# Kernel optimization log

Hardware: AMD Instinct MI355X
Metric: run time of the kernel (lower is better)

Reference implementation:

```python
import jax, jax.numpy as jnp
import numpy as np

NTYPES = 2
MAXNEI = 128      # maxNeighborNum
M2 = 16
NPER = 256        # atoms per type
B = 4
EMB = [25, 50, 100]
FIT_IN = M2 * EMB[-1]  # 1600
FH = 240


def setup_inputs() -> dict:
    key = jax.random.key(0)
    ks = jax.random.split(key, 16)
    s = 0.1
    inp = {
        "Ri": jax.random.normal(ks[0], (B, NTYPES * NPER, NTYPES * MAXNEI, 4), jnp.float32),
        "emb_W0": jax.random.normal(ks[1], (4, 1, EMB[0]), jnp.float32) * s,
        "emb_b0": jax.random.normal(ks[2], (4, EMB[0]), jnp.float32) * s,
        "emb_W1": jax.random.normal(ks[3], (4, EMB[0], EMB[1]), jnp.float32) * s,
        "emb_b1": jax.random.normal(ks[4], (4, EMB[1]), jnp.float32) * s,
        "emb_W2": jax.random.normal(ks[5], (4, EMB[1], EMB[2]), jnp.float32) * s,
        "emb_b2": jax.random.normal(ks[6], (4, EMB[2]), jnp.float32) * s,
        "fit_W0": jax.random.normal(ks[7], (2, FIT_IN, FH), jnp.float32) * 0.02,
        "fit_b0": jax.random.normal(ks[8], (2, FH), jnp.float32) * s,
        "fit_W1": jax.random.normal(ks[9], (2, FH, FH), jnp.float32) * 0.05,
        "fit_b1": jax.random.normal(ks[10], (2, FH), jnp.float32) * s,
        "fit_W2": jax.random.normal(ks[11], (2, FH, FH), jnp.float32) * 0.05,
        "fit_b2": jax.random.normal(ks[12], (2, FH), jnp.float32) * s,
        "fit_W3": jax.random.normal(ks[13], (2, FH, 1), jnp.float32) * 0.05,
        "fit_b3": jax.random.normal(ks[14], (2, 1), jnp.float32),
    }
    return inp


def _emb(s, W0, b0, W1, b1, W2, b2):
    # DeepMD-style embedding MLP with doubling resnet skips (1->25->50->100)
    h0 = jnp.tanh(s @ W0 + b0)
    h1 = jnp.tanh(h0 @ W1 + b1) + jnp.concatenate([h0, h0], axis=-1)
    h2 = jnp.tanh(h1 @ W2 + b2) + jnp.concatenate([h1, h1], axis=-1)
    return h2


def _fit(d, W0, b0, W1, b1, W2, b2, W3, b3):
    h = jnp.tanh(d @ W0 + b0)
    h = jnp.tanh(h @ W1 + b1) + h   # resnet skip (equal dims)
    h = jnp.tanh(h @ W2 + b2) + h
    return h @ W3 + b3              # [B, N, 1]


def reference(Ri, emb_W0, emb_b0, emb_W1, emb_b1, emb_W2, emb_b2,
              fit_W0, fit_b0, fit_W1, fit_b1, fit_W2, fit_b2, fit_W3, fit_b3):
    type_nums = NTYPES
    Ei_blocks = []
    for i in range(NTYPES):                      # center-atom type
        Ri_i = Ri[:, i * NPER:(i + 1) * NPER]    # [B, NPER, NTYPES*M, 4]
        xyz = None
        for j in range(NTYPES):                  # neighbor type
            blk = Ri_i[:, :, j * MAXNEI:(j + 1) * MAXNEI, :]  # [B,N,M,4]
            S = blk[..., 0:1]                                  # [B,N,M,1]
            e = i * NTYPES + j
            G = _emb(S, emb_W0[e], emb_b0[e], emb_W1[e], emb_b1[e],
                     emb_W2[e], emb_b2[e])                     # [B,N,M,100]
            tmp = jnp.einsum('bnmc,bnmg->bncg', blk, G)        # [B,N,4,100]
            xyz = tmp if xyz is None else xyz + tmp
        xyz = xyz / (MAXNEI * type_nums)
        xyz_b = xyz[..., :M2]                                  # [B,N,4,16]
        DR = jnp.einsum('bncg,bnch->bngh', xyz, xyz_b)         # [B,N,100,16]
        DR = DR.reshape(B, NPER, FIT_IN)
        Ei_i = _fit(DR, fit_W0[i], fit_b0[i], fit_W1[i], fit_b1[i],
                    fit_W2[i], fit_b2[i], fit_W3[i], fit_b3[i])  # [B,N,1]
        Ei_blocks.append(Ei_i)
    Ei = jnp.concatenate(Ei_blocks, axis=1)     # [B, natoms_sum, 1]
    return Ei[..., 0]                            # per-atom energies [B, natoms_sum]
```

## Files before the change

### kernel.cpp

```cpp
#include <hip/hip_runtime.h>
#include <hip/hip_bf16.h>

#define FH 240
#define FIT_IN 1600
#define NK 2048
#define TLO -16.0f
#define TINVH 64.0f
#define KSPLIT0 8
#define CHUNK0 200

typedef _Float16 h8 __attribute__((ext_vector_type(8)));
typedef float f4v __attribute__((ext_vector_type(4)));

__device__ __forceinline__ float fast_tanh(float x) {
    float e2 = __builtin_amdgcn_exp2f(x * 2.8853900817779268f);
    return 1.0f - 2.0f * __builtin_amdgcn_rcpf(e2 + 1.0f);
}

#define FMA_ROW(r, s) \
    acc[r][0] += (s) * b0.x; acc[r][1] += (s) * b0.y; \
    acc[r][2] += (s) * b0.z; acc[r][3] += (s) * b0.w; \
    acc[r][4] += (s) * b1.x; acc[r][5] += (s) * b1.y; \
    acc[r][6] += (s) * b1.z; acc[r][7] += (s) * b1.w;

#define TOFF_W0   0
#define TOFF_B0   28
#define TOFF_B1   56
#define TOFF_B2   108
#define TOFF_W1   208
#define TOFF_W2   1508
#define TOFF_H0T  6708
#define TOFF_H1T  10008
#define TSMEM     16608

__global__ __launch_bounds__(256) void k_prep(
    const float* __restrict__ eW0, const float* __restrict__ eB0,
    const float* __restrict__ eW1, const float* __restrict__ eB1,
    const float* __restrict__ eW2, const float* __restrict__ eB2,
    float* __restrict__ T,
    const float* __restrict__ fW0, const float* __restrict__ fW1,
    const float* __restrict__ fW2,
    _Float16* __restrict__ W0T, _Float16* __restrict__ W1T,
    _Float16* __restrict__ W2T)
{
    __shared__ float sm[TSMEM];
    const int t = threadIdx.x;

    if (blockIdx.x >= 64) {
        const int bid0 = blockIdx.x - 64;
        const int total = 768000 + 115200 + 115200;
        for (int idx = bid0 * 256 + t; idx < total; idx += 448 * 256) {
            if (idx < 768000) {
                const int tp = idx / 384000, r = idx - tp * 384000;
                const int n = r / 1600, k = r - n * 1600;
                W0T[idx] = (_Float16)fW0[tp * 384000 + k * 240 + n];
            } else if (idx < 883200) {
                const int j = idx - 768000;
                const int tp = j / 57600, r = j - tp * 57600;
                const int n = r / 240, k = r - n * 240;
                W1T[j] = (_Float16)fW1[tp * 57600 + k * 240 + n];
            } else {
                const int j = idx - 883200;
                const int tp = j / 57600, r = j - tp * 57600;
                const int n = r / 240, k = r - n * 240;
                W2T[j] = (_Float16)fW2[tp * 57600 + k * 240 + n];
            }
        }
        return;
    }

    const int w    = t >> 6;
    const int lane = t & 63;
    const int mi   = lane & 7;
    const int gi   = lane >> 3;
    const int mrow = w * 32 + mi * 4;

    const int e  = blockIdx.x >> 4;
    const int k0 = (blockIdx.x & 15) * 128;

    for (int idx = t; idx < 1250; idx += 256) {
        int k = idx / 50, g = idx - k * 50;
        sm[TOFF_W1 + k * 52 + g] = eW1[e * 1250 + idx];
    }
    for (int idx = t; idx < 5000; idx += 256) {
        int k = idx / 100, r = idx - k * 100;
        int half = r / 50, g = r - half * 50;
        sm[TOFF_W2 + k * 104 + half * 52 + g] = eW2[e * 5000 + idx];
    }
    if (t < 25)       { sm[TOFF_W0 + t] = eW0[e * 25 + t]; sm[TOFF_B0 + t] = eB0[e * 25 + t]; }
    else if (t < 75)  { sm[TOFF_B1 + (t - 25)] = eB1[e * 50 + (t - 25)]; }
    else if (t < 175) { sm[TOFF_B2 + (t - 75)] = eB2[e * 100 + (t - 75)]; }
    __syncthreads();

    if (t < 128) {
        const float S = TLO + (float)(k0 + t) * (1.0f / TINVH);
        #pragma unroll
        for (int k = 0; k < 25; ++k)
            sm[TOFF_H0T + k * 132 + t] = fast_tanh(S * sm[TOFF_W0 + k] + sm[TOFF_B0 + k]);
    }
    __syncthreads();

    {
        float acc[4][8];
        #pragma unroll
        for (int r = 0; r < 4; ++r)
            #pragma unroll
            for (int c = 0; c < 8; ++c) acc[r][c] = 0.f;

        #pragma unroll 5
        for (int k = 0; k < 25; ++k) {
            const float4 av = *(const float4*)&sm[TOFF_H0T + k * 132 + mrow];
            const float4 b0 = *(const float4*)&sm[TOFF_W1 + k * 52 + gi * 8];
            const float4 b1 = *(const float4*)&sm[TOFF_W1 + k * 52 + gi * 8 + 4];
            FMA_ROW(0, av.x) FMA_ROW(1, av.y) FMA_ROW(2, av.z) FMA_ROW(3, av.w)
        }
        #pragma unroll
        for (int c = 0; c < 8; ++c) {
            const int g = gi * 8 + c;
            if (g < 50) {
                const int gm = (g < 25) ? g : g - 25;
                const float4 h0r = *(const float4*)&sm[TOFF_H0T + gm * 132 + mrow];
                const float bias = sm[TOFF_B1 + g];
                float4 o;
                o.x = fast_tanh(acc[0][c] + bias) + h0r.x;
                o.y = fast_tanh(acc[1][c] + bias) + h0r.y;
                o.z = fast_tanh(acc[2][c] + bias) + h0r.z;
                o.w = fast_tanh(acc[3][c] + bias) + h0r.w;
                *(float4*)&sm[TOFF_H1T + g * 132 + mrow] = o;
            }
        }
    }
    __syncthreads();

    for (int half = 0; half < 2; ++half) {
        float acc[4][8];
        #pragma unroll
        for (int r = 0; r < 4; ++r)
            #pragma unroll
            for (int c = 0; c < 8; ++c) acc[r][c] = 0.f;

        #pragma unroll 5
        for (int k = 0; k < 50; ++k) {
            const float4 av = *(const float4*)&sm[TOFF_H1T + k * 132 + mrow];
            const float4 b0 = *(const float4*)&sm[TOFF_W2 + k * 104 + half * 52 + gi * 8];
            const float4 b1 = *(const float4*)&sm[TOFF_W2 + k * 104 + half * 52 + gi * 8 + 4];
            FMA_ROW(0, av.x) FMA_ROW(1, av.y) FMA_ROW(2, av.z) FMA_ROW(3, av.w)
        }
        #pragma unroll
        for (int c = 0; c < 8; ++c) {
            const int g = gi * 8 + c;
            if (g < 50) {
                const float4 h1r = *(const float4*)&sm[TOFF_H1T + g * 132 + mrow];
                const float bias = sm[TOFF_B2 + half * 50 + g];
                float* out = T + ((size_t)e * NK + k0 + mrow) * 100 + half * 50 + g;
                out[0]   = fast_tanh(acc[0][c] + bias) + h1r.x;
                out[100] = fast_tanh(acc[1][c] + bias) + h1r.y;
                out[200] = fast_tanh(acc[2][c] + bias) + h1r.z;
                out[300] = fast_tanh(acc[3][c] + bias) + h1r.w;
            }
        }
    }
}

__global__ __launch_bounds__(256) void k_xyz(
    const float* __restrict__ Ri, const float* __restrict__ T,
    _Float16* __restrict__ DRh)
{
    __shared__ float4 sR[256];
    __shared__ float  sF[256];
    __shared__ int    sI[256];
    __shared__ float  sXYZ[400];

    const int t   = threadIdx.x;
    const int blk = blockIdx.x;
    const int b   = blk >> 9;
    const int i   = (blk >> 8) & 1;
    const int n   = blk & 255;

    for (int idx = t; idx < 400; idx += 256) sXYZ[idx] = 0.f;

    {
        const int jj = t >> 7, m = t & 127;
        const size_t row = ((size_t)(b * 512 + i * 256 + n)) * 256 + jj * 128 + m;
        const float4 r = *(const float4*)(Ri + row * 4);
        sR[t] = r;
        float u = (r.x - TLO) * TINVH;
        int ii = (int)u;
        ii = (ii < 0) ? 0 : ((ii > NK - 2) ? NK - 2 : ii);
        sI[t] = ii;
        sF[t] = u - (float)ii;
    }
    __syncthreads();

    const int jj = t >> 7;
    const int g  = t & 127;
    if (g < 100) {
        const float* Te = T + ((size_t)(i * 2 + jj)) * NK * 100 + g;
        float a0 = 0.f, a1 = 0.f, a2 = 0.f, a3 = 0.f;
        #pragma unroll 4
        for (int m = 0; m < 128; ++m) {
            const int s = jj * 128 + m;
            const float4 R = sR[s];
            const float  f = sF[s];
            const float* p = Te + (size_t)sI[s] * 100;
            const float v0 = p[0], v1 = p[100];
            const float G = v0 + f * (v1 - v0);
            a0 += R.x * G; a1 += R.y * G; a2 += R.z * G; a3 += R.w * G;
        }
        atomicAdd(&sXYZ[g],       a0);
        atomicAdd(&sXYZ[100 + g], a1);
        atomicAdd(&sXYZ[200 + g], a2);
        atomicAdd(&sXYZ[300 + g], a3);
    }
    __syncthreads();

    const float inv = 1.0f / 65536.0f;
    _Float16* dr = DRh + (((size_t)i * 4 + b) * 256 + n) * FIT_IN;
    for (int q = t; q < 400; q += 256) {
        const int gg = q >> 2, h0 = (q & 3) * 4;
        ushort4 pk;
        _Float16* ph = (_Float16*)&pk;
        #pragma unroll
        for (int r = 0; r < 4; ++r) {
            const int h = h0 + r;
            const float v = (sXYZ[gg] * sXYZ[h] + sXYZ[100 + gg] * sXYZ[100 + h]
                           + sXYZ[200 + gg] * sXYZ[200 + h] + sXYZ[300 + gg] * sXYZ[300 + h]) * inv;
            ph[r] = (_Float16)v;
        }
        *(ushort4*)(dr + gg * 16 + h0) = pk;
    }
}

template<int K, int CHUNK>
__global__ __launch_bounds__(256) void k_fit_mfma(
    const _Float16* __restrict__ A, const _Float16* __restrict__ WT,
    float* __restrict__ P)
{
    __shared__ _Float16 sA[64 * 40];
    __shared__ _Float16 sBT[240 * 40];

    const int t    = threadIdx.x;
    const int w    = t >> 6;
    const int lane = t & 63;
    const int ln   = lane & 15;
    const int quad = lane >> 4;

    const int mtile = blockIdx.x;
    const int ks    = blockIdx.y;
    const int row0  = mtile * 64;
    const int tp    = mtile >> 4;
    const int kbeg  = ks * CHUNK;
    const int kend  = (kbeg + CHUNK < K) ? (kbeg + CHUNK) : K;
    const int nf0   = w * 4;
    const int nfrags = (w < 3) ? 4 : 3;

    f4v acc[4][4];
    #pragma unroll
    for (int mf = 0; mf < 4; ++mf)
        #pragma unroll
        for (int nf = 0; nf < 4; ++nf) acc[mf][nf] = (f4v)0.f;

    const _Float16* Ab = A + (size_t)row0 * K;
    const _Float16* Wb = WT + (size_t)tp * 240 * K;

    for (int k0 = kbeg; k0 < kend; k0 += 32) {
        #pragma unroll
        for (int q = t; q < 512; q += 256) {
            const int m = q >> 3, kq = (q & 7) * 4;
            const int k = k0 + kq;
            uint2 v = make_uint2(0u, 0u);
            if (k < kend) v = *(const uint2*)(Ab + (size_t)m * K + k);
            *(uint2*)&sA[m * 40 + kq] = v;
        }
        for (int q = t; q < 1920; q += 256) {
            const int n = q >> 3, kq = (q & 7) * 4;
            const int k = k0 + kq;
            uint2 v = make_uint2(0u, 0u);
            if (k < kend) v = *(const uint2*)(Wb + (size_t)n * K + k);
            *(uint2*)&sBT[n * 40 + kq] = v;
        }
        __syncthreads();

        h8 afr[4];
        #pragma unroll
        for (int mf = 0; mf < 4; ++mf)
            afr[mf] = *(const h8*)&sA[(mf * 16 + ln) * 40 + quad * 8];
        #pragma unroll
        for (int nf = 0; nf < 4; ++nf) {
            if (nf < nfrags) {
                const h8 bfr = *(const h8*)&sBT[((nf0 + nf) * 16 + ln) * 40 + quad * 8];
                #pragma unroll
                for (int mf = 0; mf < 4; ++mf)
                    acc[mf][nf] = __builtin_amdgcn_mfma_f32_16x16x32_f16(
                        afr[mf], bfr, acc[mf][nf], 0, 0, 0);
            }
        }
        __syncthreads();
    }

    float* Pb = P + ((size_t)ks * 2048 + row0) * FH;
    #pragma unroll
    for (int nf = 0; nf < 4; ++nf) {
        if (nf < nfrags) {
            const int col = (nf0 + nf) * 16 + ln;
            #pragma unroll
            for (int mf = 0; mf < 4; ++mf)
                #pragma unroll
                for (int r = 0; r < 4; ++r) {
                    const int row = mf * 16 + quad * 4 + r;
                    Pb[(size_t)row * FH + col] = acc[mf][nf][r];
                }
        }
    }
}

__global__ __launch_bounds__(256) void k_fit_tail(
    const float* __restrict__ P,
    const _Float16* __restrict__ W1T, const _Float16* __restrict__ W2T,
    const float* __restrict__ fb0, const float* __restrict__ fb1,
    const float* __restrict__ fb2, const float* __restrict__ fW3,
    const float* __restrict__ fb3, float* __restrict__ out)
{
    __shared__ float    hRes[2][16 * 240];
    __shared__ _Float16 sA[16 * 264];
    __shared__ _Float16 sB[240 * 40];

    const int t    = threadIdx.x;
    const int w    = t >> 6;
    const int lane = t & 63;
    const int ln   = lane & 15;
    const int quad = lane >> 4;
    const int r0   = blockIdx.x * 16;
    const int tp   = r0 >> 10;
    const int nf0  = w * 4;
    const int nfrags = (w < 3) ? 4 : 3;

    #pragma unroll
    for (int j = 0; j < 15; ++j) {
        const int e = t + j * 256;
        const int m = e / 240, col = e - m * 240;
        const size_t base = (size_t)(r0 + m) * FH + col;
        float s = 0.f;
        #pragma unroll
        for (int ks = 0; ks < KSPLIT0; ++ks)
            s += P[(size_t)ks * 2048 * FH + base];
        const float v = fast_tanh(s + fb0[tp * FH + col]);
        hRes[0][m * 240 + col] = v;
        sA[m * 264 + col] = (_Float16)v;
    }
    if (t < 256) {
        const int m = t >> 4, c = 240 + (t & 15);
        sA[m * 264 + c] = (_Float16)0.f;
    }

    #pragma unroll
    for (int layer = 0; layer < 2; ++layer) {
        const _Float16* Wt = (layer == 0 ? W1T : W2T) + (size_t)tp * FH * FH;
        const float* Bias  = (layer == 0 ? fb1 : fb2) + tp * FH;
        const float* res   = hRes[layer];
        float* outb        = hRes[layer ^ 1];

        f4v acc[4];
        #pragma unroll
        for (int nf = 0; nf < 4; ++nf) acc[nf] = (f4v)0.f;

        for (int k0 = 0; k0 < 256; k0 += 32) {
            __syncthreads();
            for (int q = t; q < 1920; q += 256) {
                const int n = q >> 3, kq = (q & 7) * 4;
                const int k = k0 + kq;
                uint2 v = make_uint2(0u, 0u);
                if (k < FH) v = *(const uint2*)(Wt + (size_t)n * FH + k);
                *(uint2*)&sB[n * 40 + kq] = v;
            }
            __syncthreads();
            const h8 afr = *(const h8*)&sA[ln * 264 + k0 + quad * 8];
            #pragma unroll
            for (int nf = 0; nf < 4; ++nf) {
                if (nf < nfrags) {
                    const h8 bfr = *(const h8*)&sB[((nf0 + nf) * 16 + ln) * 40 + quad * 8];
                    acc[nf] = __builtin_amdgcn_mfma_f32_16x16x32_f16(afr, bfr, acc[nf], 0, 0, 0);
                }
            }
        }
        __syncthreads();

        #pragma unroll
        for (int nf = 0; nf < 4; ++nf) {
            if (nf < nfrags) {
                const int col = (nf0 + nf) * 16 + ln;
                const float bias = Bias[col];
                #pragma unroll
                for (int r = 0; r < 4; ++r) {
                    const int m = quad * 4 + r;
                    const float v = fast_tanh(acc[nf][r] + bias) + res[m * 240 + col];
                    outb[m * 240 + col] = v;
                    if (layer == 0) sA[m * 264 + col] = (_Float16)v;
                }
            }
        }
        __syncthreads();
    }

    const float* h2 = hRes[0];
    const float* wv = fW3 + tp * FH;
    #pragma unroll
    for (int rr = 0; rr < 4; ++rr) {
        const int m = w * 4 + rr;
        float s = 0.f;
        for (int k = lane; k < FH; k += 64)
            s += h2[m * 240 + k] * wv[k];
        #pragma unroll
        for (int off = 32; off > 0; off >>= 1) s += __shfl_down(s, off);
        if (lane == 0) {
            const int gr = r0 + m;
            const int b = (gr >> 8) & 3, n = gr & 255;
            out[b * 512 + tp * 256 + n] = s + fb3[tp];
        }
    }
}

extern "C" void kernel_launch(void* const* d_in, const int* in_sizes, int n_in,
                              void* d_out, int out_size, void* d_ws, size_t ws_size,
                              hipStream_t stream)
{
    const float* Ri  = (const float*)d_in[0];
    const float* eW0 = (const float*)d_in[1];
    const float* eB0 = (const float*)d_in[2];
    const float* eW1 = (const float*)d_in[3];
    const float* eB1 = (const float*)d_in[4];
    const float* eW2 = (const float*)d_in[5];
    const float* eB2 = (const float*)d_in[6];
    const float* fW0 = (const float*)d_in[7];
    const float* fb0 = (const float*)d_in[8];
    const float* fW1 = (const float*)d_in[9];
    const float* fb1 = (const float*)d_in[10];
    const float* fW2 = (const float*)d_in[11];
    const float* fb2 = (const float*)d_in[12];
    const float* fW3 = (const float*)d_in[13];
    const float* fb3 = (const float*)d_in[14];

    char* p = (char*)d_ws;
    float* T   = (float*)p;                 p += (size_t)4 * NK * 100 * 4;
    float* P   = (float*)p;                 p += (size_t)KSPLIT0 * 2048 * FH * 4;
    _Float16* DRh = (_Float16*)p;           p += (size_t)2048 * FIT_IN * 2;
    _Float16* W0T = (_Float16*)p;           p += (size_t)768000 * 2;
    _Float16* W1T = (_Float16*)p;           p += (size_t)115200 * 2;
    _Float16* W2T = (_Float16*)p;           p += (size_t)115200 * 2;

    k_prep<<<dim3(512), dim3(256), 0, stream>>>(eW0, eB0, eW1, eB1, eW2, eB2, T,
                                                fW0, fW1, fW2, W0T, W1T, W2T);
    k_xyz<<<dim3(2048), dim3(256), 0, stream>>>(Ri, T, DRh);

    k_fit_mfma<FIT_IN, CHUNK0><<<dim3(32, KSPLIT0), dim3(256), 0, stream>>>(DRh, W0T, P);

    k_fit_tail<<<dim3(128), dim3(256), 0, stream>>>(P, W1T, W2T, fb0, fb1, fb2, fW3, fb3,
                                                    (float*)d_out);
}
```

Measured before the change: 190.6 us.

## Stage whole K-chunk in LDS for fit GEMM and restructure tail layers

The first fitting-layer GEMM now loads its entire K chunk (96 wide) of activations and weights into shared memory once and then runs all MFMAs with no per-step barriers, with the split-K factor raised to 17 to keep the grid wide. The tail kernel stages weight rows in 64-row panels covering the full K dimension, so each wave computes one 16-column fragment over all of K. It also double-buffers the fp16 activations and keeps a single in-place fp32 residual. This trades fewer barriers and load phases for more LDS use and more partial-sum buffers for the tail to reduce.

```diff
diff --git a/kernel.cpp b/kernel.cpp
--- a/kernel.cpp
+++ b/kernel.cpp
@@ -6,8 +6,8 @@
 #define NK 2048
 #define TLO -16.0f
 #define TINVH 64.0f
-#define KSPLIT0 8
-#define CHUNK0 200
+#define KSPLIT0 17
+#define CHUNK0 96
 
 typedef _Float16 h8 __attribute__((ext_vector_type(8)));
 typedef float f4v __attribute__((ext_vector_type(4)));
@@ -231,13 +231,12 @@
     }
 }
 
-template<int K, int CHUNK>
 __global__ __launch_bounds__(256) void k_fit_mfma(
     const _Float16* __restrict__ A, const _Float16* __restrict__ WT,
     float* __restrict__ P)
 {
-    __shared__ _Float16 sA[64 * 40];
-    __shared__ _Float16 sBT[240 * 40];
+    __shared__ _Float16 sW[240 * 104];
+    __shared__ _Float16 sA[64 * 104];
 
     const int t    = threadIdx.x;
     const int w    = t >> 6;
@@ -249,10 +248,26 @@
     const int ks    = blockIdx.y;
     const int row0  = mtile * 64;
     const int tp    = mtile >> 4;
-    const int kbeg  = ks * CHUNK;
-    const int kend  = (kbeg + CHUNK < K) ? (kbeg + CHUNK) : K;
+    const int kbeg  = ks * CHUNK0;
+    const int kend  = (kbeg + CHUNK0 < FIT_IN) ? (kbeg + CHUNK0) : FIT_IN;
+    const int klen  = kend - kbeg;
     const int nf0   = w * 4;
     const int nfrags = (w < 3) ? 4 : 3;
+
+    const _Float16* Ab = A + (size_t)row0 * FIT_IN + kbeg;
+    const _Float16* Wb = WT + (size_t)tp * 240 * FIT_IN + kbeg;
+
+    for (int q = t; q < 240 * 24; q += 256) {
+        const int n = q / 24, kq = (q - n * 24) * 4;
+        if (kq < klen)
+            *(uint2*)&sW[n * 104 + kq] = *(const uint2*)(Wb + (size_t)n * FIT_IN + kq);
+    }
+    for (int q = t; q < 64 * 24; q += 256) {
+        const int m = q / 24, kq = (q - m * 24) * 4;
+        if (kq < klen)
+            *(uint2*)&sA[m * 104 + kq] = *(const uint2*)(Ab + (size_t)m * FIT_IN + kq);
+    }
+    __syncthreads();
 
     f4v acc[4][4];
     #pragma unroll
@@ -260,42 +275,21 @@
         #pragma unroll
         for (int nf = 0; nf < 4; ++nf) acc[mf][nf] = (f4v)0.f;
 
-    const _Float16* Ab = A + (size_t)row0 * K;
-    const _Float16* Wb = WT + (size_t)tp * 240 * K;
-
-    for (int k0 = kbeg; k0 < kend; k0 += 32) {
-        #pragma unroll
-        for (int q = t; q < 512; q += 256) {
-            const int m = q >> 3, kq = (q & 7) * 4;
-            const int k = k0 + kq;
-            uint2 v = make_uint2(0u, 0u);
-            if (k < kend) v = *(const uint2*)(Ab + (size_t)m * K + k);
-            *(uint2*)&sA[m * 40 + kq] = v;
-        }
-        for (int q = t; q < 1920; q += 256) {
-            const int n = q >> 3, kq = (q & 7) * 4;
-            const int k = k0 + kq;
-            uint2 v = make_uint2(0u, 0u);
-            if (k < kend) v = *(const uint2*)(Wb + (size_t)n * K + k);
-            *(uint2*)&sBT[n * 40 + kq] = v;
-        }
-        __syncthreads();
-
+    for (int k0 = 0; k0 < klen; k0 += 32) {
         h8 afr[4];
         #pragma unroll
         for (int mf = 0; mf < 4; ++mf)
-            afr[mf] = *(const h8*)&sA[(mf * 16 + ln) * 40 + quad * 8];
+            afr[mf] = *(const h8*)&sA[(mf * 16 + ln) * 104 + k0 + quad * 8];
         #pragma unroll
         for (int nf = 0; nf < 4; ++nf) {
             if (nf < nfrags) {
-                const h8 bfr = *(const h8*)&sBT[((nf0 + nf) * 16 + ln) * 40 + quad * 8];
+                const h8 bfr = *(const h8*)&sW[((nf0 + nf) * 16 + ln) * 104 + k0 + quad * 8];
                 #pragma unroll
                 for (int mf = 0; mf < 4; ++mf)
                     acc[mf][nf] = __builtin_amdgcn_mfma_f32_16x16x32_f16(
                         afr[mf], bfr, acc[mf][nf], 0, 0, 0);
             }
         }
-        __syncthreads();
     }
 
     float* Pb = P + ((size_t)ks * 2048 + row0) * FH;
@@ -321,9 +315,9 @@
     const float* __restrict__ fb2, const float* __restrict__ fW3,
     const float* __restrict__ fb3, float* __restrict__ out)
 {
-    __shared__ float    hRes[2][16 * 240];
-    __shared__ _Float16 sA[16 * 264];
-    __shared__ _Float16 sB[240 * 40];
+    __shared__ _Float16 sStage[64 * 248];
+    __shared__ _Float16 sAbuf[2][16 * 264];
+    __shared__ float    hRes[16 * 240];
 
     const int t    = threadIdx.x;
     const int w    = t >> 6;
@@ -332,8 +326,12 @@
     const int quad = lane >> 4;
     const int r0   = blockIdx.x * 16;
     const int tp   = r0 >> 10;
-    const int nf0  = w * 4;
-    const int nfrags = (w < 3) ? 4 : 3;
+
+    for (int q = t; q < 2 * 16 * 264; q += 256) ((_Float16*)sAbuf)[q] = (_Float16)0.f;
+    if (t < 128) {
+        const int n = t >> 1, kq = 240 + (t & 1) * 4;
+        *(uint2*)&sStage[n * 248 + kq] = make_uint2(0u, 0u);
+    }
 
     #pragma unroll
     for (int j = 0; j < 15; ++j) {
@@ -345,71 +343,57 @@
         for (int ks = 0; ks < KSPLIT0; ++ks)
             s += P[(size_t)ks * 2048 * FH + base];
         const float v = fast_tanh(s + fb0[tp * FH + col]);
-        hRes[0][m * 240 + col] = v;
-        sA[m * 264 + col] = (_Float16)v;
-    }
-    if (t < 256) {
-        const int m = t >> 4, c = 240 + (t & 15);
-        sA[m * 264 + c] = (_Float16)0.f;
-    }
-
-    #pragma unroll
+        hRes[m * 240 + col] = v;
+        sAbuf[0][m * 264 + col] = (_Float16)v;
+    }
+
     for (int layer = 0; layer < 2; ++layer) {
         const _Float16* Wt = (layer == 0 ? W1T : W2T) + (size_t)tp * FH * FH;
         const float* Bias  = (layer == 0 ? fb1 : fb2) + tp * FH;
-        const float* res   = hRes[layer];
-        float* outb        = hRes[layer ^ 1];
-
-        f4v acc[4];
-        #pragma unroll
-        for (int nf = 0; nf < 4; ++nf) acc[nf] = (f4v)0.f;
-
-        for (int k0 = 0; k0 < 256; k0 += 32) {
+        const _Float16* inA = sAbuf[layer];
+        _Float16* outA      = sAbuf[layer ^ 1];
+
+        for (int p = 0; p < 4; ++p) {
             __syncthreads();
-            for (int q = t; q < 1920; q += 256) {
-                const int n = q >> 3, kq = (q & 7) * 4;
-                const int k = k0 + kq;
-                uint2 v = make_uint2(0u, 0u);
-                if (k < FH) v = *(const uint2*)(Wt + (size_t)n * FH + k);
-                *(uint2*)&sB[n * 40 + kq] = v;
+            const int nrows = (p < 3) ? 64 : 48;
+            for (int q = t; q < 64 * 60; q += 256) {
+                const int n = q / 60, kq = (q - n * 60) * 4;
+                if (n < nrows)
+                    *(uint2*)&sStage[n * 248 + kq] =
+                        *(const uint2*)(Wt + (size_t)(p * 64 + n) * FH + kq);
             }
             __syncthreads();
-            const h8 afr = *(const h8*)&sA[ln * 264 + k0 + quad * 8];
-            #pragma unroll
-            for (int nf = 0; nf < 4; ++nf) {
-                if (nf < nfrags) {
-                    const h8 bfr = *(const h8*)&sB[((nf0 + nf) * 16 + ln) * 40 + quad * 8];
-                    acc[nf] = __builtin_amdgcn_mfma_f32_16x16x32_f16(afr, bfr, acc[nf], 0, 0, 0);
+
+            const int f = p * 4 + w;
+            if (f < 15) {
+                f4v acc = (f4v)0.f;
+                #pragma unroll
+                for (int s = 0; s < 8; ++s) {
+                    const h8 afr = *(const h8*)&inA[ln * 264 + s * 32 + quad * 8];
+                    const h8 bfr = *(const h8*)&sStage[(w * 16 + ln) * 248 + s * 32 + quad * 8];
+                    acc = __builtin_amdgcn_mfma_f32_16x16x32_f16(afr, bfr, acc, 0, 0, 0);
                 }
-            }
-        }
-        __syncthreads();
-
-        #pragma unroll
-        for (int nf = 0; nf < 4; ++nf) {
-            if (nf < nfrags) {
-                const int col = (nf0 + nf) * 16 + ln;
+                const int col = f * 16 + ln;
                 const float bias = Bias[col];
                 #pragma unroll
                 for (int r = 0; r < 4; ++r) {
                     const int m = quad * 4 + r;
-                    const float v = fast_tanh(acc[nf][r] + bias) + res[m * 240 + col];
-                    outb[m * 240 + col] = v;
-                    if (layer == 0) sA[m * 264 + col] = (_Float16)v;
+                    const float v = fast_tanh(acc[r] + bias) + hRes[m * 240 + col];
+                    hRes[m * 240 + col] = v;
+                    outA[m * 264 + col] = (_Float16)v;
                 }
             }
         }
-        __syncthreads();
-    }
-
-    const float* h2 = hRes[0];
+    }
+    __syncthreads();
+
     const float* wv = fW3 + tp * FH;
     #pragma unroll
     for (int rr = 0; rr < 4; ++rr) {
         const int m = w * 4 + rr;
         float s = 0.f;
         for (int k = lane; k < FH; k += 64)
-            s += h2[m * 240 + k] * wv[k];
+            s += hRes[m * 240 + k] * wv[k];
         #pragma unroll
         for (int off = 32; off > 0; off >>= 1) s += __shfl_down(s, off);
         if (lane == 0) {
@@ -452,7 +436,7 @@
                                                 fW0, fW1, fW2, W0T, W1T, W2T);
     k_xyz<<<dim3(2048), dim3(256), 0, stream>>>(Ri, T, DRh);
 
-    k_fit_mfma<FIT_IN, CHUNK0><<<dim3(32, KSPLIT0), dim3(256), 0, stream>>>(DRh, W0T, P);
+    k_fit_mfma<<<dim3(32, KSPLIT0), dim3(256), 0, stream>>>(DRh, W0T, P);
 
     k_fit_tail<<<dim3(128), dim3(256), 0, stream>>>(P, W1T, W2T, fb0, fb1, fb2, fW3, fb3,
                                                     (float*)d_out);
```

After: 213.4 us. +12.0%, slower.
